# Kernel optimization log

Measured on AMD Instinct MI355X. Metric: run time of the kernel, lower is better.

Reference implementation:

```python
import jax, jax.numpy as jnp
import numpy as np

B, NS, F_IN, H, DEG = 128, 200, 200, 128, 64
N = B * NS
E = B * NS * DEG


def leaky_relu(v):
    return jnp.where(v > 0, v, 0.01 * v)


def gcn_conv(x, W, b, src, dst, w_pos):
    # PyG GCNConv with add_self_loops=True (self-loop weight 1) and
    # symmetric deg^{-1/2} normalization; aggregation flows src -> dst.
    n = x.shape[0]
    deg = jax.ops.segment_sum(w_pos, dst, num_segments=n) + 1.0  # +1 from self-loop
    dinv = jnp.where(deg > 0, deg ** -0.5, 0.0)
    norm = dinv[src] * w_pos * dinv[dst]          # [E]
    xw = x @ W                                     # [N,H]
    msg = norm[:, None] * xw[src]                  # [E,H]
    out = jax.ops.segment_sum(msg, dst, num_segments=n)
    out = out + (dinv * dinv)[:, None] * xw        # self-loop: norm = deg^{-1}
    return out + b


def setup_inputs() -> dict:
    key = jax.random.key(0)
    ks = jax.random.split(key, 14)
    # edges: each node gets DEG incoming edges from random nodes in SAME graph
    src_local = jax.random.randint(ks[0], (B, NS * DEG), 0, NS)
    dst_local = jnp.tile(jnp.repeat(jnp.arange(NS), DEG)[None, :], (B, 1))
    offsets = (jnp.arange(B) * NS)[:, None]
    src = (src_local + offsets).reshape(-1).astype(jnp.int32)
    dst = (dst_local + offsets).reshape(-1).astype(jnp.int32)
    edge_index = jnp.stack([src, dst])             # [2,E]
    edge_weight = jax.random.normal(ks[1], (E,), dtype=jnp.float32)  # mixed sign
    x = jax.random.normal(ks[2], (N, F_IN), dtype=jnp.float32)
    s = 0.05
    p = {
        'W0': jax.random.normal(ks[3], (F_IN, H)) * s, 'b0': jnp.zeros((H,)),
        'W1': jax.random.normal(ks[4], (H, H)) * s,    'b1': jnp.zeros((H,)),
        'W2': jax.random.normal(ks[5], (H, H)) * s,    'b2': jnp.zeros((H,)),
        'lincomb_W': jax.random.normal(ks[6], (NS * H, H)) * 0.01,
        'lincomb_b': jnp.zeros((H,)),
        'fc1_W': jax.random.normal(ks[7], (H, H // 2)) * s, 'fc1_b': jnp.zeros((H // 2,)),
        'fc2_W': jax.random.normal(ks[8], (H // 2, H // 4)) * s, 'fc2_b': jnp.zeros((H // 4,)),
        'fc3_W': jax.random.normal(ks[9], (H // 4, 1)) * s, 'fc3_b': jnp.zeros((1,)),
    }
    return {'x': x, 'edge_index': edge_index, 'edge_weight': edge_weight, **p}


def reference(x, edge_index, edge_weight,
              W0, b0, W1, b1, W2, b2,
              lincomb_W, lincomb_b,
              fc1_W, fc1_b, fc2_W, fc2_b, fc3_W, fc3_b):
    src, dst = edge_index[0], edge_index[1]
    # convert_edge_positive: dropping non-positive edges == zeroing their weight
    w_pos = jnp.where(edge_weight > 0, edge_weight, 0.0)
    h = gcn_conv(x, W0, b0, src, dst, w_pos)
    h = leaky_relu(h)
    h = gcn_conv(h, W1, b1, src, dst, w_pos)
    h = leaky_relu(h)
    h = gcn_conv(h, W2, b2, src, dst, w_pos)  # no activation on last layer
    # per-graph flatten + lincomb
    g = h.reshape(B, NS * H) @ lincomb_W + lincomb_b   # [B,H]
    g = leaky_relu(g @ fc1_W + fc1_b)
    g = leaky_relu(g @ fc2_W + fc2_b)
    out = g @ fc3_W + fc3_b                            # [B,1]
    return out
```

## Files before the change

### kernel.cpp

```cpp
#include <hip/hip_runtime.h>

#define B_GRAPHS 128
#define NSN      200
#define F_INPUT  200
#define HDIM     128
#define DEG      64
#define N_NODES  (B_GRAPHS * NSN)
#define E_EDGES  (N_NODES * DEG)

__global__ __launch_bounds__(256) void k_dinv(const float* __restrict__ ew,
                                              float* __restrict__ dinv) {
  const int node = blockIdx.x * 4 + (threadIdx.x >> 6);
  const int lane = threadIdx.x & 63;
  float w = ew[(size_t)node * DEG + lane];
  w = w > 0.f ? w : 0.f;
  #pragma unroll
  for (int off = 32; off > 0; off >>= 1) w += __shfl_down(w, off);
  if (lane == 0) dinv[node] = rsqrtf(w + 1.0f);
}

__global__ __launch_bounds__(256) void k_norm(const int* __restrict__ src,
                                              const int* __restrict__ dst,
                                              const float* __restrict__ ew,
                                              const float* __restrict__ dinv,
                                              float* __restrict__ nrm) {
  const int e = blockIdx.x * 256 + threadIdx.x;
  float w = ew[e];
  w = w > 0.f ? w : 0.f;
  nrm[e] = dinv[src[e]] * w * dinv[dst[e]];
}

template <int F>
__global__ __launch_bounds__(256) void k_gemm(const float* __restrict__ X,
                                              const float* __restrict__ W,
                                              float* __restrict__ out) {
  __shared__ float Xs[64][8];
  __shared__ float Ws[8][128];
  const int t  = threadIdx.x;
  const int tx = t & 31;
  const int ty = t >> 5;
  const size_t row0 = (size_t)blockIdx.x * 64;
  float acc[8][4] = {};
  for (int k0 = 0; k0 < F; k0 += 8) {
    {
      const int i = t * 2;
      const int r = i >> 3, kk = i & 7;
      const float2 v = *reinterpret_cast<const float2*>(X + (row0 + r) * F + (k0 + kk));
      Xs[r][kk] = v.x; Xs[r][kk + 1] = v.y;
    }
    {
      const int j = t * 4;
      const int kk = j >> 7, col = j & 127;
      const float4 v = *reinterpret_cast<const float4*>(W + (size_t)(k0 + kk) * HDIM + col);
      *reinterpret_cast<float4*>(&Ws[kk][col]) = v;
    }
    __syncthreads();
    float xr[8][8];
    #pragma unroll
    for (int ii = 0; ii < 8; ++ii) {
      const float4 a = *reinterpret_cast<const float4*>(&Xs[ty * 8 + ii][0]);
      const float4 b = *reinterpret_cast<const float4*>(&Xs[ty * 8 + ii][4]);
      xr[ii][0] = a.x; xr[ii][1] = a.y; xr[ii][2] = a.z; xr[ii][3] = a.w;
      xr[ii][4] = b.x; xr[ii][5] = b.y; xr[ii][6] = b.z; xr[ii][7] = b.w;
    }
    #pragma unroll
    for (int kk = 0; kk < 8; ++kk) {
      const float4 wq = *reinterpret_cast<const float4*>(&Ws[kk][tx * 4]);
      const float wv[4] = {wq.x, wq.y, wq.z, wq.w};
      #pragma unroll
      for (int ii = 0; ii < 8; ++ii)
        #pragma unroll
        for (int jj = 0; jj < 4; ++jj)
          acc[ii][jj] = fmaf(xr[ii][kk], wv[jj], acc[ii][jj]);
    }
    __syncthreads();
  }
  #pragma unroll
  for (int ii = 0; ii < 8; ++ii) {
    const float4 v = {acc[ii][0], acc[ii][1], acc[ii][2], acc[ii][3]};
    *reinterpret_cast<float4*>(out + (row0 + ty * 8 + ii) * HDIM + tx * 4) = v;
  }
}

__global__ __launch_bounds__(512) void k_agg(const float* __restrict__ xw,
                                             const int* __restrict__ src,
                                             const float* __restrict__ nrm,
                                             const float* __restrict__ dinv,
                                             const float* __restrict__ bias,
                                             float* __restrict__ out,
                                             const int leaky) {
  __shared__ float xs[NSN * HDIM];
  const int g    = blockIdx.x >> 1;
  const int half = blockIdx.x & 1;
  const int t    = threadIdx.x;
  const int w    = t >> 6;
  const int lane = t & 63;

  {
    const float4* s4 = reinterpret_cast<const float4*>(xw + (size_t)g * NSN * HDIM);
    float4* d4 = reinterpret_cast<float4*>(xs);
    for (int i = t; i < NSN * HDIM / 4; i += 512) d4[i] = s4[i];
  }
  __syncthreads();

  const float2 bv = *reinterpret_cast<const float2*>(bias + lane * 2);
  const float2* xs2 = reinterpret_cast<const float2*>(xs);

  for (int nloc = half * 100 + w; nloc < half * 100 + 100; nloc += 8) {
    const int ng = g * NSN + nloc;
    const int   s_k = src[(size_t)ng * DEG + lane] - g * NSN;
    const float n_k = nrm[(size_t)ng * DEG + lane];
    float ax = 0.f, ay = 0.f;
    #pragma unroll
    for (int k = 0; k < DEG; ++k) {
      const int   s  = __shfl(s_k, k);
      const float nv = __shfl(n_k, k);
      const float2 v = xs2[s * (HDIM / 2) + lane];
      ax = fmaf(nv, v.x, ax);
      ay = fmaf(nv, v.y, ay);
    }
    const float di = dinv[ng];
    const float sc = di * di;
    const float2 xv = xs2[nloc * (HDIM / 2) + lane];
    ax = fmaf(sc, xv.x, ax) + bv.x;
    ay = fmaf(sc, xv.y, ay) + bv.y;
    if (leaky) {
      ax = ax > 0.f ? ax : 0.01f * ax;
      ay = ay > 0.f ? ay : 0.01f * ay;
    }
    *reinterpret_cast<float2*>(out + (size_t)ng * HDIM + lane * 2) = make_float2(ax, ay);
  }
}

__global__ __launch_bounds__(256) void k_lincomb(const float* __restrict__ h,
                                                 const float* __restrict__ Wl,
                                                 float* __restrict__ P) {
  const int i = blockIdx.x;
  __shared__ float As[128][8];
  __shared__ float Bs[8][128];
  const int t   = threadIdx.x;
  const int txx = t & 15;
  const int ty  = t >> 4;
  float acc[8][8] = {};
  for (int k0 = 0; k0 < HDIM; k0 += 8) {
    {
      const int idx = t * 4;
      const int r = idx >> 3, kk = idx & 7;
      const float4 v = *reinterpret_cast<const float4*>(
          h + ((size_t)r * NSN + i) * HDIM + k0 + kk);
      As[r][kk] = v.x; As[r][kk + 1] = v.y; As[r][kk + 2] = v.z; As[r][kk + 3] = v.w;
    }
    {
      const int idx = t * 4;
      const int kk = idx >> 7, col = idx & 127;
      const float4 v = *reinterpret_cast<const float4*>(
          Wl + ((size_t)i * HDIM + k0 + kk) * HDIM + col);
      *reinterpret_cast<float4*>(&Bs[kk][col]) = v;
    }
    __syncthreads();
    #pragma unroll
    for (int kk = 0; kk < 8; ++kk) {
      float av[8], bv[8];
      #pragma unroll
      for (int ii = 0; ii < 8; ++ii) av[ii] = As[ty * 8 + ii][kk];
      #pragma unroll
      for (int jj = 0; jj < 8; ++jj) bv[jj] = Bs[kk][txx + jj * 16];
      #pragma unroll
      for (int ii = 0; ii < 8; ++ii)
        #pragma unroll
        for (int jj = 0; jj < 8; ++jj)
          acc[ii][jj] = fmaf(av[ii], bv[jj], acc[ii][jj]);
    }
    __syncthreads();
  }
  #pragma unroll
  for (int ii = 0; ii < 8; ++ii)
    #pragma unroll
    for (int jj = 0; jj < 8; ++jj)
      P[((size_t)i * B_GRAPHS + ty * 8 + ii) * HDIM + txx + jj * 16] = acc[ii][jj];
}

__global__ __launch_bounds__(256) void k_reduce(const float* __restrict__ P,
                                                const float* __restrict__ bl,
                                                float* __restrict__ g) {
  const int idx = blockIdx.x * 256 + threadIdx.x;
  float s0 = 0.f, s1 = 0.f, s2 = 0.f, s3 = 0.f;
  #pragma unroll 4
  for (int i = 0; i < NSN; i += 4) {
    s0 += P[(size_t)(i + 0) * (B_GRAPHS * HDIM) + idx];
    s1 += P[(size_t)(i + 1) * (B_GRAPHS * HDIM) + idx];
    s2 += P[(size_t)(i + 2) * (B_GRAPHS * HDIM) + idx];
    s3 += P[(size_t)(i + 3) * (B_GRAPHS * HDIM) + idx];
  }
  g[idx] = (s0 + s1) + (s2 + s3) + bl[idx & 127];
}

__global__ __launch_bounds__(64) void k_fc(const float* __restrict__ g,
                                           const float* __restrict__ f1W,
                                           const float* __restrict__ f1b,
                                           const float* __restrict__ f2W,
                                           const float* __restrict__ f2b,
                                           const float* __restrict__ f3W,
                                           const float* __restrict__ f3b,
                                           float* __restrict__ out) {
  const int b = blockIdx.x, t = threadIdx.x;
  __shared__ float gb[128];
  __shared__ float a1[64];
  __shared__ float a2[32];
  gb[t]      = g[(size_t)b * HDIM + t];
  gb[t + 64] = g[(size_t)b * HDIM + t + 64];
  __syncthreads();
  float acc = f1b[t];
  #pragma unroll 8
  for (int c = 0; c < 128; ++c) acc = fmaf(gb[c], f1W[c * 64 + t], acc);
  a1[t] = acc > 0.f ? acc : 0.01f * acc;
  __syncthreads();
  if (t < 32) {
    float a = f2b[t];
    #pragma unroll 8
    for (int c = 0; c < 64; ++c) a = fmaf(a1[c], f2W[c * 32 + t], a);
    a2[t] = a > 0.f ? a : 0.01f * a;
  }
  __syncthreads();
  if (t == 0) {
    float a = f3b[0];
    #pragma unroll
    for (int c = 0; c < 32; ++c) a = fmaf(a2[c], f3W[c], a);
    out[b] = a;
  }
}

extern "C" void kernel_launch(void* const* d_in, const int* in_sizes, int n_in,
                              void* d_out, int out_size, void* d_ws, size_t ws_size,
                              hipStream_t stream) {
  const float* x   = (const float*)d_in[0];
  const int*   ei  = (const int*)  d_in[1];
  const float* ew  = (const float*)d_in[2];
  const float* W0  = (const float*)d_in[3];
  const float* b0  = (const float*)d_in[4];
  const float* W1  = (const float*)d_in[5];
  const float* b1  = (const float*)d_in[6];
  const float* W2  = (const float*)d_in[7];
  const float* b2  = (const float*)d_in[8];
  const float* Wl  = (const float*)d_in[9];
  const float* bl  = (const float*)d_in[10];
  const float* f1W = (const float*)d_in[11];
  const float* f1b = (const float*)d_in[12];
  const float* f2W = (const float*)d_in[13];
  const float* f2b = (const float*)d_in[14];
  const float* f3W = (const float*)d_in[15];
  const float* f3b = (const float*)d_in[16];
  float* out = (float*)d_out;

  const int* src = ei;
  const int* dst = ei + E_EDGES;

  float* dinv = (float*)d_ws;
  float* nrm  = dinv + 32768;
  float* xw   = nrm + E_EDGES;
  float* hA   = xw + (size_t)N_NODES * HDIM;
  float* hB   = hA + (size_t)N_NODES * HDIM;
  float* P    = hB;
  float* g    = hB + (size_t)N_NODES * HDIM;

  k_dinv<<<N_NODES / 4, 256, 0, stream>>>(ew, dinv);
  k_norm<<<E_EDGES / 256, 256, 0, stream>>>(src, dst, ew, dinv, nrm);

  k_gemm<F_INPUT><<<N_NODES / 64, 256, 0, stream>>>(x, W0, xw);
  k_agg<<<B_GRAPHS * 2, 512, 0, stream>>>(xw, src, nrm, dinv, b0, hA, 1);
  k_gemm<HDIM><<<N_NODES / 64, 256, 0, stream>>>(hA, W1, xw);
  k_agg<<<B_GRAPHS * 2, 512, 0, stream>>>(xw, src, nrm, dinv, b1, hB, 1);
  k_gemm<HDIM><<<N_NODES / 64, 256, 0, stream>>>(hB, W2, xw);
  k_agg<<<B_GRAPHS * 2, 512, 0, stream>>>(xw, src, nrm, dinv, b2, hA, 0);

  k_lincomb<<<NSN, 256, 0, stream>>>(hA, Wl, P);
  k_reduce<<<(B_GRAPHS * HDIM) / 256, 256, 0, stream>>>(P, bl, g);
  k_fc<<<B_GRAPHS, 64, 0, stream>>>(g, f1W, f1b, f2W, f2b, f3W, f3b, out);
}
```

Baseline: 374.0 us.

## Compact positive-weight edges per node and skip zero-weight edges in aggregation

A prep kernel replaces the normalization pass. It uses a wave ballot to compact each node's positive-weight edges to the front, stores graph-local source indices and norms, and records a padded count. The aggregation loop then runs only to that count, using readlane instead of shuffles, which skips roughly half the gathers for edges whose weight is clamped to zero. Buffer aliasing also drops the hB workspace by reusing hA and xw. The risk is a loop with a dynamic trip count in place of the fully unrolled fixed loop.

```diff
diff --git a/kernel.cpp b/kernel.cpp
--- a/kernel.cpp
+++ b/kernel.cpp
@@ -19,15 +19,35 @@
   if (lane == 0) dinv[node] = rsqrtf(w + 1.0f);
 }
 
-__global__ __launch_bounds__(256) void k_norm(const int* __restrict__ src,
-                                              const int* __restrict__ dst,
+__global__ __launch_bounds__(256) void k_prep(const int* __restrict__ src,
                                               const float* __restrict__ ew,
                                               const float* __restrict__ dinv,
-                                              float* __restrict__ nrm) {
-  const int e = blockIdx.x * 256 + threadIdx.x;
-  float w = ew[e];
-  w = w > 0.f ? w : 0.f;
-  nrm[e] = dinv[src[e]] * w * dinv[dst[e]];
+                                              int* __restrict__ csrc,
+                                              float* __restrict__ cnrm,
+                                              int* __restrict__ cntp) {
+  const int node = blockIdx.x * 4 + (threadIdx.x >> 6);
+  const int lane = threadIdx.x & 63;
+  const int g = node / NSN;
+  const size_t e = (size_t)node * DEG + lane;
+  const float w = ew[e];
+  const int s = src[e];
+  const bool act = w > 0.f;
+  float nv = act ? dinv[s] * w * dinv[node] : 0.f;
+  const unsigned long long m = __ballot(act);
+  const unsigned long long below = (lane == 63) ? ~0ull >> 1
+                                                : ((1ull << lane) - 1ull);
+  const int cnt = __popcll(m);
+  const size_t base = (size_t)node * DEG;
+  if (act) {
+    const int pos = __popcll(m & below);
+    csrc[base + pos] = s - g * NSN;
+    cnrm[base + pos] = nv;
+  } else {
+    const int rank = __popcll(~m & below);
+    csrc[base + cnt + rank] = 0;
+    cnrm[base + cnt + rank] = 0.f;
+  }
+  if (lane == 0) cntp[node] = (cnt + 3) & ~3;
 }
 
 template <int F>
@@ -83,8 +103,9 @@
 }
 
 __global__ __launch_bounds__(512) void k_agg(const float* __restrict__ xw,
-                                             const int* __restrict__ src,
-                                             const float* __restrict__ nrm,
+                                             const int* __restrict__ csrc,
+                                             const float* __restrict__ cnrm,
+                                             const int* __restrict__ cntp,
                                              const float* __restrict__ dinv,
                                              const float* __restrict__ bias,
                                              float* __restrict__ out,
@@ -108,16 +129,21 @@
 
   for (int nloc = half * 100 + w; nloc < half * 100 + 100; nloc += 8) {
     const int ng = g * NSN + nloc;
-    const int   s_k = src[(size_t)ng * DEG + lane] - g * NSN;
-    const float n_k = nrm[(size_t)ng * DEG + lane];
+    const size_t base = (size_t)ng * DEG;
+    const int   s_k = csrc[base + lane];
+    const float n_k = cnrm[base + lane];
+    const int  kmax = cntp[ng];
     float ax = 0.f, ay = 0.f;
-    #pragma unroll
-    for (int k = 0; k < DEG; ++k) {
-      const int   s  = __shfl(s_k, k);
-      const float nv = __shfl(n_k, k);
-      const float2 v = xs2[s * (HDIM / 2) + lane];
-      ax = fmaf(nv, v.x, ax);
-      ay = fmaf(nv, v.y, ay);
+    for (int k = 0; k < kmax; k += 4) {
+      #pragma unroll
+      for (int j = 0; j < 4; ++j) {
+        const int   s  = __builtin_amdgcn_readlane(s_k, k + j);
+        const float nv = __uint_as_float(
+            __builtin_amdgcn_readlane(__float_as_uint(n_k), k + j));
+        const float2 v = xs2[s * (HDIM / 2) + lane];
+        ax = fmaf(nv, v.x, ax);
+        ay = fmaf(nv, v.y, ay);
+      }
     }
     const float di = dinv[ng];
     const float sc = di * di;
@@ -253,25 +279,25 @@
   float* out = (float*)d_out;
 
   const int* src = ei;
-  const int* dst = ei + E_EDGES;
 
   float* dinv = (float*)d_ws;
-  float* nrm  = dinv + 32768;
-  float* xw   = nrm + E_EDGES;
+  int*   csrc = (int*)(dinv + 32768);
+  float* cnrm = (float*)(csrc + E_EDGES);
+  int*   cntp = (int*)(cnrm + E_EDGES);
+  float* xw   = (float*)(cntp + 32768);
   float* hA   = xw + (size_t)N_NODES * HDIM;
-  float* hB   = hA + (size_t)N_NODES * HDIM;
-  float* P    = hB;
-  float* g    = hB + (size_t)N_NODES * HDIM;
+  float* P    = xw;
+  float* g    = hA + (size_t)N_NODES * HDIM;
 
   k_dinv<<<N_NODES / 4, 256, 0, stream>>>(ew, dinv);
-  k_norm<<<E_EDGES / 256, 256, 0, stream>>>(src, dst, ew, dinv, nrm);
+  k_prep<<<N_NODES / 4, 256, 0, stream>>>(src, ew, dinv, csrc, cnrm, cntp);
 
   k_gemm<F_INPUT><<<N_NODES / 64, 256, 0, stream>>>(x, W0, xw);
-  k_agg<<<B_GRAPHS * 2, 512, 0, stream>>>(xw, src, nrm, dinv, b0, hA, 1);
+  k_agg<<<B_GRAPHS * 2, 512, 0, stream>>>(xw, csrc, cnrm, cntp, dinv, b0, hA, 1);
   k_gemm<HDIM><<<N_NODES / 64, 256, 0, stream>>>(hA, W1, xw);
-  k_agg<<<B_GRAPHS * 2, 512, 0, stream>>>(xw, src, nrm, dinv, b1, hB, 1);
-  k_gemm<HDIM><<<N_NODES / 64, 256, 0, stream>>>(hB, W2, xw);
-  k_agg<<<B_GRAPHS * 2, 512, 0, stream>>>(xw, src, nrm, dinv, b2, hA, 0);
+  k_agg<<<B_GRAPHS * 2, 512, 0, stream>>>(xw, csrc, cnrm, cntp, dinv, b1, hA, 1);
+  k_gemm<HDIM><<<N_NODES / 64, 256, 0, stream>>>(hA, W2, xw);
+  k_agg<<<B_GRAPHS * 2, 512, 0, stream>>>(xw, csrc, cnrm, cntp, dinv, b2, hA, 0);
 
   k_lincomb<<<NSN, 256, 0, stream>>>(hA, Wl, P);
   k_reduce<<<(B_GRAPHS * HDIM) / 256, 256, 0, stream>>>(P, bl, g);
```

Measured after the change: 323.6 us. -13.5%, faster.
